# Kernel tuning notes

Hardware: AMD Instinct MI355X
Metric: run time of the kernel (lower is better)

Reference implementation:

```python
import jax, jax.numpy as jnp
import numpy as np

BINS = 16
EDGE_KS = 11
EDGE_SIGMA = 1.5
EPS = 1e-9


def _gauss1d(ks, sigma):
    x = jnp.arange(ks, dtype=jnp.float32) - (ks - 1) / 2.0
    g = jnp.exp(-(x * x) / (2.0 * sigma * sigma))
    return g / jnp.sum(g)


def _conv2d(x, k):
    # x: [B,Cin,H,W], k: [Cout,Cin,kh,kw], VALID padding
    return jax.lax.conv_general_dilated(x, k, (1, 1), 'VALID',
                                        dimension_numbers=('NCHW', 'OIHW', 'NCHW'))


def _gaussian_blur(x, ks, sigma):
    g = _gauss1d(ks, sigma)
    k = jnp.outer(g, g)[None, None]  # [1,1,ks,ks]
    p = ks // 2
    xp = jnp.pad(x, ((0, 0), (0, 0), (p, p), (p, p)), mode='reflect')
    return _conv2d(xp, k)


# 8 neighbor offsets ordered by angle 0,45,...,315 (kornia canny convention)
_OFFS = [(0, 1), (1, 1), (1, 0), (1, -1), (0, -1), (-1, -1), (-1, 0), (-1, 1)]


def _dir_kernels(center, nbr):
    ks = np.zeros((8, 1, 3, 3), np.float32)
    for i, (dy, dx) in enumerate(_OFFS):
        ks[i, 0, 1, 1] = center
        ks[i, 0, 1 + dy, 1 + dx] = nbr
    return jnp.asarray(ks)


NMS_K = _dir_kernels(1.0, -1.0)   # center minus directional neighbor
HYST_K = _dir_kernels(0.0, 1.0)   # directional neighbor value
SOBEL = jnp.asarray(np.stack([
    np.array([[-1, 0, 1], [-2, 0, 2], [-1, 0, 1]], np.float32),
    np.array([[-1, -2, -1], [0, 0, 0], [1, 2, 1]], np.float32)])[:, None])  # [2,1,3,3]


def _canny_edges(gray, low=0.1, high=0.2):
    blurred = _gaussian_blur(gray, 5, 1.0)
    gp = jnp.pad(blurred, ((0, 0), (0, 0), (1, 1), (1, 1)), mode='edge')
    grads = _conv2d(gp, SOBEL)                       # [B,2,H,W]
    gx, gy = grads[:, :1], grads[:, 1:]
    mag = jnp.sqrt(gx * gx + gy * gy + 1e-6)
    ang = jnp.round(jnp.rad2deg(jnp.arctan2(gy, gx)) / 45.0)
    pos_i = jnp.mod(ang, 8).astype(jnp.int32)        # [B,1,H,W]
    neg_i = jnp.mod(ang + 4, 8).astype(jnp.int32)
    mp = jnp.pad(mag, ((0, 0), (0, 0), (1, 1), (1, 1)))
    nms = _conv2d(mp, NMS_K)                         # [B,8,H,W]
    pos = jnp.take_along_axis(nms, pos_i, axis=1)
    neg = jnp.take_along_axis(nms, neg_i, axis=1)
    mag = mag * (jnp.minimum(pos, neg) > 0.0)
    edges = (mag > low).astype(jnp.float32) * 0.5 + (mag > high).astype(jnp.float32) * 0.5

    def body(c):
        e, _ = c
        weak = (e == 0.5).astype(jnp.float32)
        strong = (e == 1.0).astype(jnp.float32)
        nb = _conv2d(jnp.pad(e, ((0, 0), (0, 0), (1, 1), (1, 1))), HYST_K)
        hm = jnp.any(nb == 1.0, axis=1, keepdims=True).astype(jnp.float32) * weak + strong
        return (hm + (hm == 0.0) * weak * 0.5, e)

    def cond(c):
        e, old = c
        return jnp.any(e != old)

    edges, _ = jax.lax.while_loop(cond, body, (edges, -jnp.ones_like(edges)))
    return (edges == 1.0).astype(jnp.float32)


def _normalize_map(m):
    B = m.shape[0]
    f = m.reshape(B, -1)
    mn = f.min(axis=1).reshape(B, 1, 1, 1)
    mx = f.max(axis=1).reshape(B, 1, 1, 1)
    return (m - mn) / (mx - mn + EPS)


def _srd(x_norm, mean, std, alpha, beta):
    B, C, H, W = x_norm.shape
    x = jnp.clip(x_norm * std + mean, 0.0, 1.0)
    gray = 0.299 * x[:, :1] + 0.587 * x[:, 1:2] + 0.114 * x[:, 2:3]
    edges = _canny_edges(gray)
    edge_density = _gaussian_blur(edges, EDGE_KS, EDGE_SIGMA)
    # per-image color histogram sparsity, batched via offset indices
    qc = jnp.round(x * (BINS - 1)).astype(jnp.int32)
    combined = qc[:, 0] * BINS * BINS + qc[:, 1] * BINS + qc[:, 2]   # [B,H,W]
    nbins = BINS ** 3
    flat = combined.reshape(B, -1) + (jnp.arange(B, dtype=jnp.int32) * nbins)[:, None]
    counts = jnp.zeros(B * nbins, jnp.float32).at[flat.reshape(-1)].add(1.0)
    probs = counts / float(H * W)
    sparsity = -jnp.log(probs[flat] + EPS).reshape(B, 1, H, W)
    fused = alpha * _normalize_map(edge_density) + beta * _normalize_map(sparsity)
    return jax.nn.sigmoid(fused)


def setup_inputs():
    key = jax.random.key(0)
    x_norm = jax.random.normal(key, (16, 3, 512, 512), jnp.float32)
    mean = jnp.array([0.485, 0.456, 0.406], jnp.float32).reshape(1, 3, 1, 1)
    std = jnp.array([0.229, 0.224, 0.225], jnp.float32).reshape(1, 3, 1, 1)
    return {'x_norm': x_norm, 'mean': mean, 'std': std,
            'alpha': jnp.float32(1.0), 'beta': jnp.float32(1.0)}


def reference(x_norm, mean, std, alpha, beta):
    return _srd(x_norm, mean, std, alpha, beta)
```

## Files before the change

### kernel.cpp

```cpp
#include <hip/hip_runtime.h>
#include <stdint.h>

#define NB 16
#define HH 512
#define WW 512
#define HW (HH*WW)
#define NBINS 4096

typedef unsigned long long u64;

__device__ __forceinline__ float clip01(float v){ return fminf(fmaxf(v, 0.0f), 1.0f); }
__device__ __forceinline__ int refl(int i, int n){ if (i < 0) i = -i; if (i >= n) i = 2*n - 2 - i; return i; }
__device__ __forceinline__ int clampi(int i, int lo, int hi){ return i < lo ? lo : (i > hi ? hi : i); }

__global__ void k_zero(uint4* __restrict__ hist4){
  int idx = blockIdx.x * 256 + threadIdx.x;
  hist4[idx] = make_uint4(0u, 0u, 0u, 0u);
}

__global__ void k_prep(const float* __restrict__ x, const float* __restrict__ mean,
                       const float* __restrict__ stdv, float* __restrict__ gray,
                       uint16_t* __restrict__ comb, uint32_t* __restrict__ hist)
{
#pragma clang fp contract(off)
  __shared__ uint32_t h[NBINS];
  for (int i = threadIdx.x; i < NBINS; i += 256) h[i] = 0u;
  __syncthreads();
  int img  = blockIdx.x >> 6;
  int base = (blockIdx.x & 63) * 4096;
  float m0 = mean[0], m1 = mean[1], m2 = mean[2];
  float s0 = stdv[0], s1 = stdv[1], s2 = stdv[2];
  const float* xb = x + (size_t)img * 3 * HW;
  float*     gb   = gray + (size_t)img*HW;
  uint16_t*  cb   = comb + (size_t)img*HW;
  #pragma unroll
  for (int it = 0; it < 4; it++){
    int f4 = it*256 + threadIdx.x;
    int p  = base + f4*4;
    float4 r = *(const float4*)(xb + p);
    float4 g = *(const float4*)(xb + HW + p);
    float4 b = *(const float4*)(xb + 2*HW + p);
    float xr[4] = {r.x, r.y, r.z, r.w};
    float xg[4] = {g.x, g.y, g.z, g.w};
    float xbl[4] = {b.x, b.y, b.z, b.w};
    float gy[4]; uint16_t cc[4];
    #pragma unroll
    for (int j = 0; j < 4; j++){
      float cr = clip01(xr[j]*s0 + m0);
      float cg = clip01(xg[j]*s1 + m1);
      float cbv= clip01(xbl[j]*s2 + m2);
      gy[j] = 0.299f*cr + 0.587f*cg + 0.114f*cbv;
      int c = ((int)rintf(cr*15.0f))*256 + ((int)rintf(cg*15.0f))*16 + (int)rintf(cbv*15.0f);
      cc[j] = (uint16_t)c;
      atomicAdd(&h[c], 1u);
    }
    *(float4*)(gb + p) = make_float4(gy[0], gy[1], gy[2], gy[3]);
    ushort4 cv; cv.x = cc[0]; cv.y = cc[1]; cv.z = cc[2]; cv.w = cc[3];
    *(ushort4*)(cb + p) = cv;
  }
  __syncthreads();
  uint32_t* gh = hist + img * NBINS;
  for (int i = threadIdx.x; i < NBINS; i += 256){ uint32_t v = h[i]; if (v) atomicAdd(&gh[i], v); }
}

__global__ void k_spb(const uint32_t* __restrict__ hist, uint32_t* __restrict__ stats){
  int img = blockIdx.x;
  uint32_t mx = 0u, mn = 0xFFFFFFFFu;
  for (int i = threadIdx.x; i < NBINS; i += 256){
    uint32_t c = hist[img*NBINS + i];
    if (c > mx) mx = c;
    if (c > 0u && c < mn) mn = c;
  }
  __shared__ uint32_t rmx[256], rmn[256];
  rmx[threadIdx.x] = mx; rmn[threadIdx.x] = mn;
  __syncthreads();
  for (int s = 128; s > 0; s >>= 1){
    if (threadIdx.x < (unsigned)s){
      rmx[threadIdx.x] = max(rmx[threadIdx.x], rmx[threadIdx.x + s]);
      rmn[threadIdx.x] = min(rmn[threadIdx.x], rmn[threadIdx.x + s]);
    }
    __syncthreads();
  }
  if (threadIdx.x == 0){
    float sp_min = -logf((float)rmx[0] / 262144.0f + 1e-9f);
    float sp_max = -logf((float)rmn[0] / 262144.0f + 1e-9f);
    stats[img*4+2] = __float_as_uint(sp_min);
    stats[img*4+3] = __float_as_uint(sp_max);
  }
}

__global__ void __launch_bounds__(256) k_canny(const float* __restrict__ gray,
                                               u64* __restrict__ A, u64* __restrict__ Sb)
{
#pragma clang fp contract(off)
  __shared__ float ubuf[40*73];
  __shared__ float blr[36*69];
  __shared__ uint8_t sdir[32*64];
  int b = blockIdx.x;
  int img = b >> 7;
  int t = b & 127;
  int y0 = (t >> 3) << 5;
  int x0 = (t & 7) << 6;
  const float* gb = gray + (size_t)img*HW;
  int tid = threadIdx.x;
  float g5[5]; { float s=0.0f; for(int i=0;i<5;i++){ float tt=(float)i-2.0f; g5[i]=expf(-(tt*tt)/2.0f); s+=g5[i]; } for(int i=0;i<5;i++) g5[i]/=s; }
  for (int i = tid; i < 40*72; i += 256){
    int ly = i/72, lx = i - ly*72;
    int gy = refl(y0 - 4 + ly, HH);
    int gx = refl(x0 - 4 + lx, WW);
    ubuf[ly*73 + lx] = gb[gy*WW + gx];
  }
  __syncthreads();
  for (int task = tid; task < 272; task += 256){
    int lx = task % 68;
    int ly = (task / 68) * 9;
    float w[5][5];
    #pragma unroll
    for (int j = 0; j < 4; j++)
      #pragma unroll
      for (int k = 0; k < 5; k++)
        w[j][k] = ubuf[(ly+j)*73 + lx + k];
    #pragma unroll
    for (int s = 0; s < 9; s++){
      #pragma unroll
      for (int k = 0; k < 5; k++) w[4][k] = ubuf[(ly+s+4)*73 + lx + k];
      float acc = 0.0f;
      #pragma unroll
      for (int ky = 0; ky < 5; ky++)
        #pragma unroll
        for (int kx = 0; kx < 5; kx++)
          acc += (g5[ky]*g5[kx]) * w[ky][kx];
      blr[(ly+s)*69 + lx] = acc;
      #pragma unroll
      for (int j = 0; j < 4; j++)
        #pragma unroll
        for (int k = 0; k < 5; k++) w[j][k] = w[j+1][k];
    }
  }
  __syncthreads();
  for (int i = tid; i < 34*66; i += 256){
    int ly = i/66, lx = i - ly*66;
    int Y = y0 - 1 + ly, X = x0 - 1 + lx;
    float m = 0.0f;
    if (Y >= 0 && Y < HH && X >= 0 && X < WW){
      float v[3][3];
      for (int dy = 0; dy < 3; dy++){
        int Yl = clampi(Y + dy - 1, 0, HH-1) - (y0 - 2);
        for (int dx = 0; dx < 3; dx++){
          int Xl = clampi(X + dx - 1, 0, WW-1) - (x0 - 2);
          v[dy][dx] = blr[Yl*69 + Xl];
        }
      }
      float gx = (v[0][2] - v[0][0]) + 2.0f*(v[1][2] - v[1][0]) + (v[2][2] - v[2][0]);
      float gy = (v[2][0] + 2.0f*v[2][1] + v[2][2]) - (v[0][0] + 2.0f*v[0][1] + v[0][2]);
      m = sqrtf(gx*gx + gy*gy + 1e-6f);
      if (ly >= 1 && ly <= 32 && lx >= 1 && lx <= 64){
        float ax = fabsf(gx), ay = fabsf(gy);
        int d;
        if (ay <= 0.41421356237309503f*ax) d = (gx >= 0.0f) ? 0 : 4;
        else if (ay >= 2.4142135623730951f*ax) d = (gy > 0.0f) ? 2 : 6;
        else if (gx > 0.0f) d = (gy > 0.0f) ? 1 : 7;
        else d = (gy > 0.0f) ? 3 : 5;
        sdir[(ly-1)*64 + (lx-1)] = (uint8_t)d;
      }
    }
    ubuf[ly*67 + lx] = m;
  }
  __syncthreads();
  const int OY[8] = {0,1,1,1,0,-1,-1,-1};
  const int OX[8] = {1,1,0,-1,-1,-1,0,1};
  int lane = tid & 63, wv = tid >> 6;
  for (int j = 0; j < 8; j++){
    int y = j*4 + wv;
    int x = lane;
    float m = ubuf[(y+1)*67 + (x+1)];
    int d  = sdir[y*64 + x];
    int d2 = (d + 4) & 7;
    float mp = 0.0f, mn = 0.0f;
    { int yy=y+OY[d],  xx=x+OX[d];  int gy=y0+yy, gx=x0+xx; if(gy>=0&&gy<HH&&gx>=0&&gx<WW) mp = ubuf[(yy+1)*67 + (xx+1)]; }
    { int yy=y+OY[d2], xx=x+OX[d2]; int gy=y0+yy, gx=x0+xx; if(gy>=0&&gy<HH&&gx>=0&&gx<WW) mn = ubuf[(yy+1)*67 + (xx+1)]; }
    bool keep = ((m - mp) > 0.0f) && ((m - mn) > 0.0f);
    float mf = keep ? m : 0.0f;
    bool strong = mf > 0.2f;
    bool weak   = (mf > 0.1f) && !strong;
    u64 wb = __ballot(weak);
    u64 sb = __ballot(strong);
    if (lane == 0){
      int gy = y0 + y;
      A [img*4096 + gy*8 + (x0>>6)] = wb;
      Sb[img*4096 + gy*8 + (x0>>6)] = sb;
    }
  }
}

__device__ __forceinline__ u64 ks_flood(u64 g, u64 P){
  u64 p1 = P, g1 = g;
  g1 |= p1 & (g1 << 1);  p1 &= (p1 << 1);
  g1 |= p1 & (g1 << 2);  p1 &= (p1 << 2);
  g1 |= p1 & (g1 << 4);  p1 &= (p1 << 4);
  g1 |= p1 & (g1 << 8);  p1 &= (p1 << 8);
  g1 |= p1 & (g1 << 16); p1 &= (p1 << 16);
  g1 |= p1 & (g1 << 32);
  u64 p2 = P, g2 = g;
  g2 |= p2 & (g2 >> 1);  p2 &= (p2 >> 1);
  g2 |= p2 & (g2 >> 2);  p2 &= (p2 >> 2);
  g2 |= p2 & (g2 >> 4);  p2 &= (p2 >> 4);
  g2 |= p2 & (g2 >> 8);  p2 &= (p2 >> 8);
  g2 |= p2 & (g2 >> 16); p2 &= (p2 >> 16);
  g2 |= p2 & (g2 >> 32);
  return g1 | g2;
}

#define HROW(m, l, r_) ((m) | ((m)<<1) | ((m)>>1) | ((l)>>63) | ((r_)<<63))

#define UPD(i) do{ \
    u64 pend = Pr[i] & ~Sr[i]; \
    if (pend){ \
      u64 Sv = Sr[i]; \
      int r = r0 + (i); \
      u64 mu = ((i) > 0) ? Sr[(i)-1] : (r > 0   ? sS[(r-1)*9+w] : 0ull); \
      u64 md = ((i) < 3) ? Sr[(i)+1] : (r < 511 ? sS[(r+1)*9+w] : 0ull); \
      u64 lu = (left  && r > 0)   ? sS[(r-1)*9+w-1] : 0ull; \
      u64 ru = (right && r > 0)   ? sS[(r-1)*9+w+1] : 0ull; \
      u64 lm = left  ? sS[r*9+w-1] : 0ull; \
      u64 rm = right ? sS[r*9+w+1] : 0ull; \
      u64 ldn= (left  && r < 511) ? sS[(r+1)*9+w-1] : 0ull; \
      u64 rdn= (right && r < 511) ? sS[(r+1)*9+w+1] : 0ull; \
      u64 nb = HROW(mu,lu,ru) | HROW(Sv,lm,rm) | HROW(md,ldn,rdn); \
      u64 g = Sv | (Pr[i] & nb); \
      if (g != Sv){ \
        u64 ns = ks_flood(g, Pr[i]); \
        Sr[i] = ns; sS[r*9+w] = ns; changed = true; \
      } \
    } \
  } while(0)

__global__ void __launch_bounds__(1024) k_hyst(const u64* __restrict__ A, u64* __restrict__ S)
{
  __shared__ u64 sS[512*9];
  int img = blockIdx.x;
  const u64* gA = A + img * 4096;
  u64*       gS = S + img * 4096;
  int tid = threadIdx.x;
  for (int i = tid; i < 4096; i += 1024)
    sS[(i>>3)*9 + (i&7)] = gS[i];
  __syncthreads();
  int  w     = tid & 7;
  int  r0    = (tid >> 3) << 2;
  bool left  = (w > 0), right = (w < 7);
  u64 Sr[4], Pr[4];
  #pragma unroll
  for (int i = 0; i < 4; i++){
    Sr[i] = sS[(r0+i)*9 + w];
    Pr[i] = gA[(r0+i)*8 + w] | Sr[i];
  }
  for (;;){
    bool changed = false;
    #pragma unroll 1
    for (int rep = 0; rep < 2; rep++){
      #pragma unroll
      for (int i = 0; i < 4; i++) UPD(i);
      #pragma unroll
      for (int i = 3; i >= 0; i--) UPD(i);
    }
    if (!__syncthreads_or(changed ? 1 : 0)) break;
  }
  #pragma unroll
  for (int i = 0; i < 4; i++) gS[(r0+i)*8 + w] = Sr[i];
}

__global__ void __launch_bounds__(256) k_b11(const u64* __restrict__ S, float* __restrict__ out,
                                             float2* __restrict__ part)
{
#pragma clang fp contract(off)
  __shared__ u64 wds[74][3];
  __shared__ float hb[74][64];
  __shared__ float smn[4], smx[4];
  int b = blockIdx.x;
  int img = b >> 6;
  int t = b & 63;
  int y0 = (t >> 3) << 6;
  int tx = t & 7;
  int x0 = tx << 6;
  int tid = threadIdx.x;
  float g[11]; { float s=0.0f; for(int i=0;i<11;i++){ float tt=(float)i-5.0f; g[i]=expf(-(tt*tt)/4.5f); s+=g[i]; } for(int i=0;i<11;i++) g[i]/=s; }
  for (int i = tid; i < 74*3; i += 256){
    int j = i/3, widx = i - j*3;
    int gy = refl(y0 - 5 + j, HH);
    int gw = tx - 1 + widx;
    wds[j][widx] = (gw >= 0 && gw < 8) ? S[img*4096 + gy*8 + gw] : 0ull;
  }
  __syncthreads();
  for (int i = tid; i < 74*64; i += 256){
    int j = i >> 6, c = i & 63;
    float acc = 0.0f;
    for (int k = 0; k < 11; k++){
      int xx = refl(x0 + c + k - 5, WW);
      int widx = (xx >> 6) - tx + 1;
      float bv = (float)((wds[j][widx] >> (xx & 63)) & 1ull);
      acc += g[k] * bv;
    }
    hb[j][c] = acc;
  }
  __syncthreads();
  float mn = 3.4e38f, mx = -3.4e38f;
  float* ob = out + (size_t)img*HW;
  for (int i = tid; i < 4096; i += 256){
    int y = i >> 6, c = i & 63;
    float acc = 0.0f;
    for (int k = 0; k < 11; k++) acc += g[k] * hb[y + k][c];
    ob[(y0 + y)*WW + x0 + c] = acc;
    mn = fminf(mn, acc); mx = fmaxf(mx, acc);
  }
  for (int off = 32; off >= 1; off >>= 1){
    mn = fminf(mn, __shfl_down(mn, off));
    mx = fmaxf(mx, __shfl_down(mx, off));
  }
  int wv = tid >> 6, ln = tid & 63;
  if (ln == 0){ smn[wv] = mn; smx[wv] = mx; }
  __syncthreads();
  if (tid == 0){
    part[b] = make_float2(fminf(fminf(smn[0],smn[1]),fminf(smn[2],smn[3])),
                          fmaxf(fmaxf(smx[0],smx[1]),fmaxf(smx[2],smx[3])));
  }
}

__global__ void k_edred(const float2* __restrict__ part, uint32_t* __restrict__ stats){
  int img = blockIdx.x;
  int ln = threadIdx.x;
  float2 v = part[img*64 + ln];
  float mn = v.x, mx = v.y;
  for (int off = 32; off >= 1; off >>= 1){
    mn = fminf(mn, __shfl_down(mn, off));
    mx = fmaxf(mx, __shfl_down(mx, off));
  }
  if (ln == 0){
    stats[img*4+0] = __float_as_uint(mn);
    stats[img*4+1] = __float_as_uint(mx);
  }
}

__global__ void k_final(const float* __restrict__ ed, const uint16_t* __restrict__ comb,
                        const uint32_t* __restrict__ hist, const uint32_t* __restrict__ stats,
                        const float* __restrict__ alpha, const float* __restrict__ beta,
                        float* __restrict__ out)
{
#pragma clang fp contract(off)
  int idx = blockIdx.x * 256 + threadIdx.x;
  int img = idx >> 18;
  float a = alpha[0], b = beta[0];
  float mne = __uint_as_float(stats[img*4+0]);
  float mxe = __uint_as_float(stats[img*4+1]);
  float mns = __uint_as_float(stats[img*4+2]);
  float mxs = __uint_as_float(stats[img*4+3]);
  float e  = ed[idx];
  float sp = -logf((float)hist[img*NBINS + comb[idx]] / 262144.0f + 1e-9f);
  float en = (e  - mne) / (mxe - mne + 1e-9f);
  float sn = (sp - mns) / (mxs - mns + 1e-9f);
  float f  = a*en + b*sn;
  out[idx] = 1.0f / (1.0f + expf(-f));
}

extern "C" void kernel_launch(void* const* d_in, const int* in_sizes, int n_in,
                              void* d_out, int out_size, void* d_ws, size_t ws_size,
                              hipStream_t stream)
{
  const float* x     = (const float*)d_in[0];
  const float* mean  = (const float*)d_in[1];
  const float* stdv  = (const float*)d_in[2];
  const float* alpha = (const float*)d_in[3];
  const float* beta  = (const float*)d_in[4];
  float* out = (float*)d_out;

  char* ws = (char*)d_ws;
  float*    gray  = (float*)ws;
  uint16_t* comb  = (uint16_t*)(ws + (16u << 20));
  float2*   part  = (float2*)(ws + (24u << 20));
  uint32_t* hist  = (uint32_t*)(ws + (28u << 20));
  u64*      Ab    = (u64*)(ws + (28u << 20) + (1u << 18));
  u64*      Sb    = (u64*)(ws + (28u << 20) + (1u << 18) + (1u << 19));
  uint32_t* stats = (uint32_t*)(ws + (28u << 20) + (1u << 18) + (2u << 19));

  hipLaunchKernelGGL(k_zero,  dim3(64),    dim3(256), 0, stream, (uint4*)hist);
  hipLaunchKernelGGL(k_prep,  dim3(1024),  dim3(256), 0, stream, x, mean, stdv, gray, comb, hist);
  hipLaunchKernelGGL(k_spb,   dim3(NB),    dim3(256), 0, stream, hist, stats);
  hipLaunchKernelGGL(k_canny, dim3(2048),  dim3(256), 0, stream, gray, Ab, Sb);
  hipLaunchKernelGGL(k_hyst,  dim3(NB),    dim3(1024), 0, stream, Ab, Sb);
  hipLaunchKernelGGL(k_b11,   dim3(1024),  dim3(256), 0, stream, Sb, out, part);
  hipLaunchKernelGGL(k_edred, dim3(NB),    dim3(64),  0, stream, part, stats);
  hipLaunchKernelGGL(k_final, dim3(16384), dim3(256), 0, stream, out, comb, hist, stats, alpha, beta, out);
}
```

Measured before the change: 134.8 us.

## Coarsen hysteresis threads to 8 rows with wave-local iteration, merge histogram stats kernel

The hysteresis kernel now uses 512 threads, each owning 8 rows instead of 4. Each thread runs up to 32 forward/backward sweeps and checks convergence per wavefront with __any, so block-wide __syncthreads_or barriers happen less often. The separate histogram min/max kernel is folded into the edge-density reduction kernel, removing one launch. The tradeoff is less parallelism in hysteresis and more register pressure from the 8-row arrays.

```diff
diff --git a/kernel.cpp b/kernel.cpp
--- a/kernel.cpp
+++ b/kernel.cpp
@@ -63,32 +63,6 @@
   for (int i = threadIdx.x; i < NBINS; i += 256){ uint32_t v = h[i]; if (v) atomicAdd(&gh[i], v); }
 }
 
-__global__ void k_spb(const uint32_t* __restrict__ hist, uint32_t* __restrict__ stats){
-  int img = blockIdx.x;
-  uint32_t mx = 0u, mn = 0xFFFFFFFFu;
-  for (int i = threadIdx.x; i < NBINS; i += 256){
-    uint32_t c = hist[img*NBINS + i];
-    if (c > mx) mx = c;
-    if (c > 0u && c < mn) mn = c;
-  }
-  __shared__ uint32_t rmx[256], rmn[256];
-  rmx[threadIdx.x] = mx; rmn[threadIdx.x] = mn;
-  __syncthreads();
-  for (int s = 128; s > 0; s >>= 1){
-    if (threadIdx.x < (unsigned)s){
-      rmx[threadIdx.x] = max(rmx[threadIdx.x], rmx[threadIdx.x + s]);
-      rmn[threadIdx.x] = min(rmn[threadIdx.x], rmn[threadIdx.x + s]);
-    }
-    __syncthreads();
-  }
-  if (threadIdx.x == 0){
-    float sp_min = -logf((float)rmx[0] / 262144.0f + 1e-9f);
-    float sp_max = -logf((float)rmn[0] / 262144.0f + 1e-9f);
-    stats[img*4+2] = __float_as_uint(sp_min);
-    stats[img*4+3] = __float_as_uint(sp_max);
-  }
-}
-
 __global__ void __launch_bounds__(256) k_canny(const float* __restrict__ gray,
                                                u64* __restrict__ A, u64* __restrict__ Sb)
 {
@@ -219,7 +193,7 @@
       u64 Sv = Sr[i]; \
       int r = r0 + (i); \
       u64 mu = ((i) > 0) ? Sr[(i)-1] : (r > 0   ? sS[(r-1)*9+w] : 0ull); \
-      u64 md = ((i) < 3) ? Sr[(i)+1] : (r < 511 ? sS[(r+1)*9+w] : 0ull); \
+      u64 md = ((i) < 7) ? Sr[(i)+1] : (r < 511 ? sS[(r+1)*9+w] : 0ull); \
       u64 lu = (left  && r > 0)   ? sS[(r-1)*9+w-1] : 0ull; \
       u64 ru = (right && r > 0)   ? sS[(r-1)*9+w+1] : 0ull; \
       u64 lm = left  ? sS[r*9+w-1] : 0ull; \
@@ -230,43 +204,46 @@
       u64 g = Sv | (Pr[i] & nb); \
       if (g != Sv){ \
         u64 ns = ks_flood(g, Pr[i]); \
-        Sr[i] = ns; sS[r*9+w] = ns; changed = true; \
+        Sr[i] = ns; sS[r*9+w] = ns; c = true; \
       } \
     } \
   } while(0)
 
-__global__ void __launch_bounds__(1024) k_hyst(const u64* __restrict__ A, u64* __restrict__ S)
+__global__ void __launch_bounds__(512) k_hyst(const u64* __restrict__ A, u64* __restrict__ S)
 {
   __shared__ u64 sS[512*9];
   int img = blockIdx.x;
   const u64* gA = A + img * 4096;
   u64*       gS = S + img * 4096;
   int tid = threadIdx.x;
-  for (int i = tid; i < 4096; i += 1024)
+  for (int i = tid; i < 4096; i += 512)
     sS[(i>>3)*9 + (i&7)] = gS[i];
   __syncthreads();
   int  w     = tid & 7;
-  int  r0    = (tid >> 3) << 2;
+  int  r0    = (tid >> 3) << 3;
   bool left  = (w > 0), right = (w < 7);
-  u64 Sr[4], Pr[4];
+  u64 Sr[8], Pr[8];
   #pragma unroll
-  for (int i = 0; i < 4; i++){
+  for (int i = 0; i < 8; i++){
     Sr[i] = sS[(r0+i)*9 + w];
     Pr[i] = gA[(r0+i)*8 + w] | Sr[i];
   }
   for (;;){
     bool changed = false;
     #pragma unroll 1
-    for (int rep = 0; rep < 2; rep++){
-      #pragma unroll
-      for (int i = 0; i < 4; i++) UPD(i);
-      #pragma unroll
-      for (int i = 3; i >= 0; i--) UPD(i);
+    for (int it = 0; it < 32; ++it){
+      bool c = false;
+      #pragma unroll
+      for (int i = 0; i < 8; i++) UPD(i);
+      #pragma unroll
+      for (int i = 7; i >= 0; i--) UPD(i);
+      if (c) changed = true;
+      if (!__any(c ? 1 : 0)) break;
     }
     if (!__syncthreads_or(changed ? 1 : 0)) break;
   }
   #pragma unroll
-  for (int i = 0; i < 4; i++) gS[(r0+i)*8 + w] = Sr[i];
+  for (int i = 0; i < 8; i++) gS[(r0+i)*8 + w] = Sr[i];
 }
 
 __global__ void __launch_bounds__(256) k_b11(const u64* __restrict__ S, float* __restrict__ out,
@@ -325,18 +302,43 @@
   }
 }
 
-__global__ void k_edred(const float2* __restrict__ part, uint32_t* __restrict__ stats){
+__global__ void __launch_bounds__(256) k_edred(const float2* __restrict__ part,
+                                               const uint32_t* __restrict__ hist,
+                                               uint32_t* __restrict__ stats){
+  __shared__ uint32_t sx[4], sn[4];
   int img = blockIdx.x;
-  int ln = threadIdx.x;
-  float2 v = part[img*64 + ln];
-  float mn = v.x, mx = v.y;
+  int tid = threadIdx.x;
+  uint32_t mx = 0u, mn = 0xFFFFFFFFu;
+  for (int i = tid; i < NBINS; i += 256){
+    uint32_t c = hist[img*NBINS + i];
+    if (c > mx) mx = c;
+    if (c > 0u && c < mn) mn = c;
+  }
   for (int off = 32; off >= 1; off >>= 1){
-    mn = fminf(mn, __shfl_down(mn, off));
-    mx = fmaxf(mx, __shfl_down(mx, off));
-  }
-  if (ln == 0){
-    stats[img*4+0] = __float_as_uint(mn);
-    stats[img*4+1] = __float_as_uint(mx);
+    uint32_t ox = (uint32_t)__shfl_down((int)mx, off);
+    uint32_t on = (uint32_t)__shfl_down((int)mn, off);
+    if (ox > mx) mx = ox;
+    if (on < mn) mn = on;
+  }
+  int wv = tid >> 6, ln = tid & 63;
+  if (ln == 0){ sx[wv] = mx; sn[wv] = mn; }
+  float fmn = 3.4e38f, fmx = -3.4e38f;
+  if (wv == 0){
+    float2 v = part[img*64 + ln];
+    fmn = v.x; fmx = v.y;
+    for (int off = 32; off >= 1; off >>= 1){
+      fmn = fminf(fmn, __shfl_down(fmn, off));
+      fmx = fmaxf(fmx, __shfl_down(fmx, off));
+    }
+  }
+  __syncthreads();
+  if (tid == 0){
+    uint32_t MX = max(max(sx[0],sx[1]), max(sx[2],sx[3]));
+    uint32_t MN = min(min(sn[0],sn[1]), min(sn[2],sn[3]));
+    stats[img*4+0] = __float_as_uint(fmn);
+    stats[img*4+1] = __float_as_uint(fmx);
+    stats[img*4+2] = __float_as_uint(-logf((float)MX / 262144.0f + 1e-9f));
+    stats[img*4+3] = __float_as_uint(-logf((float)MN / 262144.0f + 1e-9f));
   }
 }
 
@@ -383,10 +385,9 @@
 
   hipLaunchKernelGGL(k_zero,  dim3(64),    dim3(256), 0, stream, (uint4*)hist);
   hipLaunchKernelGGL(k_prep,  dim3(1024),  dim3(256), 0, stream, x, mean, stdv, gray, comb, hist);
-  hipLaunchKernelGGL(k_spb,   dim3(NB),    dim3(256), 0, stream, hist, stats);
   hipLaunchKernelGGL(k_canny, dim3(2048),  dim3(256), 0, stream, gray, Ab, Sb);
-  hipLaunchKernelGGL(k_hyst,  dim3(NB),    dim3(1024), 0, stream, Ab, Sb);
+  hipLaunchKernelGGL(k_hyst,  dim3(NB),    dim3(512), 0, stream, Ab, Sb);
   hipLaunchKernelGGL(k_b11,   dim3(1024),  dim3(256), 0, stream, Sb, out, part);
-  hipLaunchKernelGGL(k_edred, dim3(NB),    dim3(64),  0, stream, part, stats);
+  hipLaunchKernelGGL(k_edred, dim3(NB),    dim3(256), 0, stream, part, hist, stats);
   hipLaunchKernelGGL(k_final, dim3(16384), dim3(256), 0, stream, out, comb, hist, stats, alpha, beta, out);
 }
```

Measured after the change: 138.4 us. +2.7%, slower.
